# Performance work log

Hardware: AMD Instinct MI355X
Metric: run time of the kernel (lower is better)

The kernel has to match this reference:

```python
import jax, jax.numpy as jnp
import numpy as np

B, T, D = 4096, 200, 128
K_SHORT = 5


def setup_inputs() -> dict:
    key = jax.random.key(0)
    ks = jax.random.split(key, 8)
    hist_items = jax.random.normal(ks[0], (B, T, D), dtype=jnp.float32)
    hist_mask = jax.random.randint(ks[1], (B, T), 0, 2).astype(bool)
    hist_mask = hist_mask.at[:, 0].set(True)  # avoid fully-masked rows
    hist_age_hours = jax.random.uniform(ks[2], (B, T), dtype=jnp.float32) * 168.0
    hist_popularity = jax.random.uniform(ks[3], (B, T), dtype=jnp.float32)
    s = 1.0 / float(np.sqrt(D))
    Wq = jax.random.normal(ks[4], (D, D), dtype=jnp.float32) * s
    Wk = jax.random.normal(ks[5], (D, D), dtype=jnp.float32) * s
    Wv = jax.random.normal(ks[6], (D, D), dtype=jnp.float32) * s
    gate_w = jax.random.normal(ks[7], (1, 2), dtype=jnp.float32) * 0.5
    gate_b = jnp.zeros((1,), dtype=jnp.float32)
    ln_gamma = jnp.ones((D,), dtype=jnp.float32)
    ln_beta = jnp.zeros((D,), dtype=jnp.float32)
    decay_alpha = jnp.asarray(0.05, dtype=jnp.float32)
    return {"hist_items": hist_items, "hist_mask": hist_mask,
            "hist_age_hours": hist_age_hours, "hist_popularity": hist_popularity,
            "Wq": Wq, "Wk": Wk, "Wv": Wv, "gate_w": gate_w, "gate_b": gate_b,
            "ln_gamma": ln_gamma, "ln_beta": ln_beta, "decay_alpha": decay_alpha}


def reference(hist_items, hist_mask, hist_age_hours, hist_popularity,
              Wq, Wk, Wv, gate_w, gate_b, ln_gamma, ln_beta, decay_alpha):
    dt = hist_items.dtype
    maskf = hist_mask.astype(dt)  # (B,T)
    # learnable time-decay bias
    alpha = jax.nn.softplus(decay_alpha) + 1e-6
    decay = jnp.exp(-alpha * hist_age_hours) * maskf  # (B,T)
    # masked mean of history as the single query
    mean_hist = (hist_items * maskf[..., None]).sum(1) / (maskf.sum(1, keepdims=True) + 1e-6)  # (B,D)
    q = mean_hist @ Wq.T                                # (B,D)
    k = jnp.einsum('btd,ed->bte', hist_items, Wk)       # (B,T,D)
    v = jnp.einsum('btd,ed->bte', hist_items, Wv)       # (B,T,D)
    scale = 1.0 / float(np.sqrt(hist_items.shape[-1]))
    scores = jnp.einsum('bd,btd->bt', q, k) * scale + jnp.log(decay + 1e-12)
    scores = jnp.where(hist_mask, scores, -jnp.inf)
    attn = jax.nn.softmax(scores, axis=-1)              # (B,T)
    long_term = jnp.einsum('bt,btd->bd', attn, v)       # (B,D)
    # vectorized last-K window: positions [cnt-K, cnt)
    cnt = jnp.maximum(hist_mask.sum(1), 1)              # (B,) int
    K = min(K_SHORT, hist_items.shape[1])
    ar = jnp.arange(hist_items.shape[1])[None, :]       # (1,T)
    lastk = (ar >= (cnt[:, None] - K)) & (ar < cnt[:, None])  # (B,T) bool
    lk = lastk.astype(dt)
    denom = jnp.maximum(lk.sum(1, keepdims=True), 1.0)  # (B,1)
    short_term = (hist_items * lk[..., None]).sum(1) / denom  # (B,D)
    mean_pop = (hist_popularity * lk).sum(1) / denom[:, 0]
    mean_rec = (hist_age_hours * lk).sum(1) / denom[:, 0]
    ctx = jnp.stack([mean_pop, mean_rec], axis=-1)      # (B,2)
    g = jax.nn.sigmoid(ctx @ gate_w.T + gate_b)         # (B,1)
    user = g * short_term + (1.0 - g) * long_term       # (B,D)
    # LayerNorm (eps=1e-5, biased variance, matching torch)
    mu = user.mean(-1, keepdims=True)
    var = user.var(-1, keepdims=True)
    return (user - mu) / jnp.sqrt(var + 1e-5) * ln_gamma + ln_beta
```

## Files before the change

### kernel.cpp

```cpp
#include <hip/hip_runtime.h>

#define BB 4096
#define TT 200
#define DD 128
#define KSHORT 5

__global__ void detect_mask_kernel(const unsigned* __restrict__ m, int* __restrict__ flag) {
  unsigned bad = 0;
  for (int i = threadIdx.x; i < 1024; i += 64) bad |= (m[i] > 1u) ? 1u : 0u;
  unsigned long long bl = __ballot(bad != 0u);
  if (threadIdx.x == 0) *flag = (bl != 0ULL) ? 1 : 0;
}

__global__ void precompute_A_kernel(const float* __restrict__ Wq,
                                    const float* __restrict__ Wk,
                                    float* __restrict__ A) {
  const int d = blockIdx.x, dp = threadIdx.x;
  float acc = 0.f;
#pragma unroll 8
  for (int e = 0; e < DD; ++e) acc += Wk[e * DD + d] * Wq[e * DD + dp];
  A[d * DD + dp] = acc * 0.08838834764831845f;
}

__global__ __launch_bounds__(256, 4) void k1_stats(
    const float* __restrict__ items, const void* __restrict__ maskp,
    const float* __restrict__ age, const float* __restrict__ pop,
    const float* __restrict__ gate_w, const float* __restrict__ gate_b,
    const float* __restrict__ A, const int* __restrict__ flagp,
    float* __restrict__ qkw, float* __restrict__ shortw, float* __restrict__ gw) {
  __shared__ float s_m[TT];
  __shared__ float s_pm[8 * DD];
  __shared__ float s_ps[8 * DD];
  __shared__ float s_mean[DD];
  __shared__ float s_scal[4];

  const int b = blockIdx.x, tid = threadIdx.x;
  const int lane32 = tid & 31, stream = tid >> 5;
  const int mode = *flagp;

  if (tid < TT) {
    int mk = mode ? (int)((const unsigned char*)maskp)[(size_t)b * TT + tid]
                  : ((const int*)maskp)[(size_t)b * TT + tid];
    s_m[tid] = mk ? 1.f : 0.f;
  }
  __syncthreads();

  if (tid < 64) {
    float c = 0.f;
    for (int t = tid; t < TT; t += 64) c += s_m[t];
#pragma unroll
    for (int o = 32; o > 0; o >>= 1) c += __shfl_xor(c, o);
    if (tid == 0) s_scal[0] = c;
  }
  __syncthreads();

  const float cntf = s_scal[0];
  const int cnt = max((int)(cntf + 0.5f), 1);
  const int lo = max(cnt - KSHORT, 0);
  const float dn = (float)(cnt - lo);

  const float* rowbase = items + (size_t)b * (TT * DD) + lane32 * 4;
  float4 ms = {0.f, 0.f, 0.f, 0.f}, ss = {0.f, 0.f, 0.f, 0.f};
  for (int t = stream; t < TT; t += 8) {
    const float mk = s_m[t];
    const bool inw = (t >= lo) && (t < cnt);
    if (mk > 0.f || inw) {
      float4 v = *(const float4*)(rowbase + t * DD);
      if (mk > 0.f) { ms.x += v.x; ms.y += v.y; ms.z += v.z; ms.w += v.w; }
      if (inw)      { ss.x += v.x; ss.y += v.y; ss.z += v.z; ss.w += v.w; }
    }
  }
  *(float4*)&s_pm[stream * DD + lane32 * 4] = ms;
  *(float4*)&s_ps[stream * DD + lane32 * 4] = ss;
  __syncthreads();

  if (tid < DD) {
    float am = 0.f, as = 0.f;
#pragma unroll
    for (int s = 0; s < 8; ++s) { am += s_pm[s * DD + tid]; as += s_ps[s * DD + tid]; }
    s_mean[tid] = am / (cntf + 1e-6f);
    shortw[(size_t)b * DD + tid] = as / dn;
  } else if (tid == DD) {
    float sp = 0.f, sr = 0.f;
    for (int t = lo; t < cnt; ++t) {
      sp += pop[(size_t)b * TT + t];
      sr += age[(size_t)b * TT + t];
    }
    float z = gate_w[0] * (sp / dn) + gate_w[1] * (sr / dn) + gate_b[0];
    gw[b] = 1.f / (1.f + expf(-z));
  }
  __syncthreads();

  if (tid < DD) {
    const float4* Ar = (const float4*)(A + tid * DD);
    float acc = 0.f;
#pragma unroll
    for (int j = 0; j < DD / 4; ++j) {
      float4 a4 = Ar[j];
      acc += a4.x * s_mean[4 * j] + a4.y * s_mean[4 * j + 1] +
             a4.z * s_mean[4 * j + 2] + a4.w * s_mean[4 * j + 3];
    }
    qkw[(size_t)b * DD + tid] = acc;
  }
}

__global__ __launch_bounds__(256, 4) void k2_attn(
    const float* __restrict__ items, const void* __restrict__ maskp,
    const float* __restrict__ age, const float* __restrict__ Wv,
    const float* __restrict__ gamma, const float* __restrict__ beta,
    const float* __restrict__ alpha_in, const int* __restrict__ flagp,
    const float* __restrict__ qkw, const float* __restrict__ shortw,
    const float* __restrict__ gw, float* __restrict__ out) {
  __shared__ float s_bias[TT];
  __shared__ float s_o[8 * DD];
  __shared__ float s_ml[16];
  __shared__ float s_w[DD];
  __shared__ float s_user[DD];
  __shared__ float s_scal[4];

  const int b = blockIdx.x, tid = threadIdx.x;
  const int lane32 = tid & 31, stream = tid >> 5;
  const int mode = *flagp;

  if (tid < TT) {
    int mk = mode ? (int)((const unsigned char*)maskp)[(size_t)b * TT + tid]
                  : ((const int*)maskp)[(size_t)b * TT + tid];
    const float a = age[(size_t)b * TT + tid];
    const float al = log1pf(expf(alpha_in[0])) + 1e-6f;
    s_bias[tid] = mk ? logf(expf(-al * a) + 1e-12f) : -1e30f;
  }
  __syncthreads();

  const float4 qk = *(const float4*)(qkw + (size_t)b * DD + lane32 * 4);
  const float* rowbase = items + (size_t)b * (TT * DD) + lane32 * 4;

  float m = -1e30f, l = 0.f;
  float4 o = {0.f, 0.f, 0.f, 0.f};
  for (int t = stream; t < TT; t += 8) {
    const float bb = s_bias[t];
    if (bb > -1e29f) {
      float4 v = *(const float4*)(rowbase + t * DD);
      float p = qk.x * v.x + qk.y * v.y + qk.z * v.z + qk.w * v.w;
      p += __shfl_xor(p, 1);
      p += __shfl_xor(p, 2);
      p += __shfl_xor(p, 4);
      p += __shfl_xor(p, 8);
      p += __shfl_xor(p, 16);
      const float s = p + bb;
      const float mn = fmaxf(m, s);
      const float f = __expf(m - mn), e = __expf(s - mn);
      l = l * f + e;
      o.x = o.x * f + e * v.x;
      o.y = o.y * f + e * v.y;
      o.z = o.z * f + e * v.z;
      o.w = o.w * f + e * v.w;
      m = mn;
    }
  }
  *(float4*)&s_o[stream * DD + lane32 * 4] = o;
  if (lane32 == 0) { s_ml[stream * 2] = m; s_ml[stream * 2 + 1] = l; }
  __syncthreads();

  if (tid < DD) {
    float M = s_ml[0];
#pragma unroll
    for (int s = 1; s < 8; ++s) M = fmaxf(M, s_ml[2 * s]);
    float L = 0.f, O = 0.f;
#pragma unroll
    for (int s = 0; s < 8; ++s) {
      const float f = __expf(s_ml[2 * s] - M);
      L += s_ml[2 * s + 1] * f;
      O += s_o[s * DD + tid] * f;
    }
    s_w[tid] = O / L;
  }
  __syncthreads();

  if (tid < DD) {
    const float4* Wr = (const float4*)(Wv + tid * DD);
    float acc = 0.f;
#pragma unroll
    for (int j = 0; j < DD / 4; ++j) {
      float4 a4 = Wr[j];
      acc += a4.x * s_w[4 * j] + a4.y * s_w[4 * j + 1] +
             a4.z * s_w[4 * j + 2] + a4.w * s_w[4 * j + 3];
    }
    const float g = gw[b];
    s_user[tid] = g * shortw[(size_t)b * DD + tid] + (1.f - g) * acc;
  }
  __syncthreads();

  if (tid < 64) {
    const float x0 = s_user[tid], x1 = s_user[64 + tid];
    float su = x0 + x1;
#pragma unroll
    for (int off = 32; off > 0; off >>= 1) su += __shfl_xor(su, off);
    const float mu = su * (1.f / 128.f);
    const float d0 = x0 - mu, d1 = x1 - mu;
    float s2 = d0 * d0 + d1 * d1;
#pragma unroll
    for (int off = 32; off > 0; off >>= 1) s2 += __shfl_xor(s2, off);
    if (tid == 0) {
      s_scal[0] = mu;
      s_scal[1] = 1.f / sqrtf(s2 * (1.f / 128.f) + 1e-5f);
    }
  }
  __syncthreads();

  if (tid < DD) {
    out[(size_t)b * DD + tid] =
        (s_user[tid] - s_scal[0]) * s_scal[1] * gamma[tid] + beta[tid];
  }
}

extern "C" void kernel_launch(void* const* d_in, const int* in_sizes, int n_in,
                              void* d_out, int out_size, void* d_ws, size_t ws_size,
                              hipStream_t stream) {
  const float* items  = (const float*)d_in[0];
  const void*  maskp  = d_in[1];
  const float* age    = (const float*)d_in[2];
  const float* pop    = (const float*)d_in[3];
  const float* Wq     = (const float*)d_in[4];
  const float* Wk     = (const float*)d_in[5];
  const float* Wv     = (const float*)d_in[6];
  const float* gate_w = (const float*)d_in[7];
  const float* gate_b = (const float*)d_in[8];
  const float* gamma  = (const float*)d_in[9];
  const float* beta   = (const float*)d_in[10];
  const float* alpha  = (const float*)d_in[11];

  char* ws = (char*)d_ws;
  int*   flag   = (int*)ws;
  float* A      = (float*)(ws + 256);
  float* qkw    = (float*)(ws + 256 + 65536);
  float* shortw = (float*)(ws + 256 + 65536 + 2097152);
  float* gw     = (float*)(ws + 256 + 65536 + 2 * 2097152);
  float* outp   = (float*)d_out;

  detect_mask_kernel<<<1, 64, 0, stream>>>((const unsigned*)maskp, flag);
  precompute_A_kernel<<<DD, DD, 0, stream>>>(Wq, Wk, A);
  k1_stats<<<BB, 256, 0, stream>>>(items, maskp, age, pop, gate_w, gate_b, A,
                                   flag, qkw, shortw, gw);
  k2_attn<<<BB, 256, 0, stream>>>(items, maskp, age, Wv, gamma, beta, alpha,
                                  flag, qkw, shortw, gw, outp);
}
```

Before: 635.6 us.

## Fuse stats and attention kernels into one per-row kernel with compacted indices

Merges the two per-batch-row kernels into a single kernel, so intermediate q·K weights, short-term vectors and gate values stay in shared memory instead of going through global workspace. Valid time steps are compacted into a shared index list, which removes per-step branch divergence. The softmax drops the running-max rescaling and instead multiplies exp(score) by the precomputed decay factor, replacing log/exp work. The second pass over the row is meant to hit in cache right after the first, but skipping the max subtraction risks overflow if scores get large. The atomic compaction also changes the summation order.

```diff
diff --git a/kernel.cpp b/kernel.cpp
--- a/kernel.cpp
+++ b/kernel.cpp
@@ -22,32 +22,41 @@
   A[d * DD + dp] = acc * 0.08838834764831845f;
 }
 
-__global__ __launch_bounds__(256, 4) void k1_stats(
+__global__ __launch_bounds__(256, 8) void fused_kernel(
     const float* __restrict__ items, const void* __restrict__ maskp,
     const float* __restrict__ age, const float* __restrict__ pop,
-    const float* __restrict__ gate_w, const float* __restrict__ gate_b,
+    const float* __restrict__ Wv, const float* __restrict__ gate_w,
+    const float* __restrict__ gate_b, const float* __restrict__ gamma,
+    const float* __restrict__ beta, const float* __restrict__ alpha_in,
     const float* __restrict__ A, const int* __restrict__ flagp,
-    float* __restrict__ qkw, float* __restrict__ shortw, float* __restrict__ gw) {
-  __shared__ float s_m[TT];
-  __shared__ float s_pm[8 * DD];
-  __shared__ float s_ps[8 * DD];
-  __shared__ float s_mean[DD];
+    float* __restrict__ out) {
+  __shared__ int   s_idx[TT];
+  __shared__ float s_wm[TT], s_ww[TT], s_df[TT];
+  __shared__ float s_pa[8 * DD];
+  __shared__ float s_pb[8 * DD];
+  __shared__ float s_mean[DD], s_qk[DD], s_w[DD], s_user[DD];
+  __shared__ float s_l[8];
   __shared__ float s_scal[4];
+  __shared__ int   s_n;
 
   const int b = blockIdx.x, tid = threadIdx.x;
   const int lane32 = tid & 31, stream = tid >> 5;
   const int mode = *flagp;
 
+  float mymask = 0.f, myage = 0.f;
+  if (tid == 0) s_n = 0;
   if (tid < TT) {
     int mk = mode ? (int)((const unsigned char*)maskp)[(size_t)b * TT + tid]
                   : ((const int*)maskp)[(size_t)b * TT + tid];
-    s_m[tid] = mk ? 1.f : 0.f;
+    mymask = mk ? 1.f : 0.f;
+    myage = age[(size_t)b * TT + tid];
+    s_wm[tid] = mymask;
   }
   __syncthreads();
 
   if (tid < 64) {
     float c = 0.f;
-    for (int t = tid; t < TT; t += 64) c += s_m[t];
+    for (int t = tid; t < TT; t += 64) c += s_wm[t];
 #pragma unroll
     for (int o = 32; o > 0; o >>= 1) c += __shfl_xor(c, o);
     if (tid == 0) s_scal[0] = c;
@@ -59,35 +68,48 @@
   const int lo = max(cnt - KSHORT, 0);
   const float dn = (float)(cnt - lo);
 
+  if (tid < TT) {
+    const bool inw = (tid >= lo) && (tid < cnt);
+    if (mymask > 0.f || inw) {
+      const float al = log1pf(expf(alpha_in[0])) + 1e-6f;
+      const int p = atomicAdd(&s_n, 1);
+      s_idx[p] = tid;
+      s_wm[p] = mymask;
+      s_ww[p] = inw ? 1.f : 0.f;
+      s_df[p] = (mymask > 0.f) ? (__expf(-al * myage) + 1e-12f) : 0.f;
+    }
+  }
+  __syncthreads();
+  const int n = s_n;
+
   const float* rowbase = items + (size_t)b * (TT * DD) + lane32 * 4;
   float4 ms = {0.f, 0.f, 0.f, 0.f}, ss = {0.f, 0.f, 0.f, 0.f};
-  for (int t = stream; t < TT; t += 8) {
-    const float mk = s_m[t];
-    const bool inw = (t >= lo) && (t < cnt);
-    if (mk > 0.f || inw) {
-      float4 v = *(const float4*)(rowbase + t * DD);
-      if (mk > 0.f) { ms.x += v.x; ms.y += v.y; ms.z += v.z; ms.w += v.w; }
-      if (inw)      { ss.x += v.x; ss.y += v.y; ss.z += v.z; ss.w += v.w; }
-    }
-  }
-  *(float4*)&s_pm[stream * DD + lane32 * 4] = ms;
-  *(float4*)&s_ps[stream * DD + lane32 * 4] = ss;
-  __syncthreads();
-
+  for (int i = stream; i < n; i += 8) {
+    const int t = s_idx[i];
+    const float wm = s_wm[i], ww = s_ww[i];
+    const float4 v = *(const float4*)(rowbase + t * DD);
+    ms.x += wm * v.x; ms.y += wm * v.y; ms.z += wm * v.z; ms.w += wm * v.w;
+    ss.x += ww * v.x; ss.y += ww * v.y; ss.z += ww * v.z; ss.w += ww * v.w;
+  }
+  *(float4*)&s_pa[stream * DD + lane32 * 4] = ms;
+  *(float4*)&s_pb[stream * DD + lane32 * 4] = ss;
+  __syncthreads();
+
+  float short_v = 0.f;
   if (tid < DD) {
     float am = 0.f, as = 0.f;
 #pragma unroll
-    for (int s = 0; s < 8; ++s) { am += s_pm[s * DD + tid]; as += s_ps[s * DD + tid]; }
+    for (int s = 0; s < 8; ++s) { am += s_pa[s * DD + tid]; as += s_pb[s * DD + tid]; }
     s_mean[tid] = am / (cntf + 1e-6f);
-    shortw[(size_t)b * DD + tid] = as / dn;
+    short_v = as / dn;
   } else if (tid == DD) {
     float sp = 0.f, sr = 0.f;
     for (int t = lo; t < cnt; ++t) {
       sp += pop[(size_t)b * TT + t];
       sr += age[(size_t)b * TT + t];
     }
-    float z = gate_w[0] * (sp / dn) + gate_w[1] * (sr / dn) + gate_b[0];
-    gw[b] = 1.f / (1.f + expf(-z));
+    const float z = gate_w[0] * (sp / dn) + gate_w[1] * (sr / dn) + gate_b[0];
+    s_scal[1] = 1.f / (1.f + expf(-z));
   }
   __syncthreads();
 
@@ -96,82 +118,42 @@
     float acc = 0.f;
 #pragma unroll
     for (int j = 0; j < DD / 4; ++j) {
-      float4 a4 = Ar[j];
+      const float4 a4 = Ar[j];
       acc += a4.x * s_mean[4 * j] + a4.y * s_mean[4 * j + 1] +
              a4.z * s_mean[4 * j + 2] + a4.w * s_mean[4 * j + 3];
     }
-    qkw[(size_t)b * DD + tid] = acc;
-  }
-}
-
-__global__ __launch_bounds__(256, 4) void k2_attn(
-    const float* __restrict__ items, const void* __restrict__ maskp,
-    const float* __restrict__ age, const float* __restrict__ Wv,
-    const float* __restrict__ gamma, const float* __restrict__ beta,
-    const float* __restrict__ alpha_in, const int* __restrict__ flagp,
-    const float* __restrict__ qkw, const float* __restrict__ shortw,
-    const float* __restrict__ gw, float* __restrict__ out) {
-  __shared__ float s_bias[TT];
-  __shared__ float s_o[8 * DD];
-  __shared__ float s_ml[16];
-  __shared__ float s_w[DD];
-  __shared__ float s_user[DD];
-  __shared__ float s_scal[4];
-
-  const int b = blockIdx.x, tid = threadIdx.x;
-  const int lane32 = tid & 31, stream = tid >> 5;
-  const int mode = *flagp;
-
-  if (tid < TT) {
-    int mk = mode ? (int)((const unsigned char*)maskp)[(size_t)b * TT + tid]
-                  : ((const int*)maskp)[(size_t)b * TT + tid];
-    const float a = age[(size_t)b * TT + tid];
-    const float al = log1pf(expf(alpha_in[0])) + 1e-6f;
-    s_bias[tid] = mk ? logf(expf(-al * a) + 1e-12f) : -1e30f;
-  }
-  __syncthreads();
-
-  const float4 qk = *(const float4*)(qkw + (size_t)b * DD + lane32 * 4);
-  const float* rowbase = items + (size_t)b * (TT * DD) + lane32 * 4;
-
-  float m = -1e30f, l = 0.f;
+    s_qk[tid] = acc;
+  }
+  __syncthreads();
+
+  const float4 qk = *(const float4*)&s_qk[lane32 * 4];
+  float l = 0.f;
   float4 o = {0.f, 0.f, 0.f, 0.f};
-  for (int t = stream; t < TT; t += 8) {
-    const float bb = s_bias[t];
-    if (bb > -1e29f) {
-      float4 v = *(const float4*)(rowbase + t * DD);
-      float p = qk.x * v.x + qk.y * v.y + qk.z * v.z + qk.w * v.w;
-      p += __shfl_xor(p, 1);
-      p += __shfl_xor(p, 2);
-      p += __shfl_xor(p, 4);
-      p += __shfl_xor(p, 8);
-      p += __shfl_xor(p, 16);
-      const float s = p + bb;
-      const float mn = fmaxf(m, s);
-      const float f = __expf(m - mn), e = __expf(s - mn);
-      l = l * f + e;
-      o.x = o.x * f + e * v.x;
-      o.y = o.y * f + e * v.y;
-      o.z = o.z * f + e * v.z;
-      o.w = o.w * f + e * v.w;
-      m = mn;
-    }
-  }
-  *(float4*)&s_o[stream * DD + lane32 * 4] = o;
-  if (lane32 == 0) { s_ml[stream * 2] = m; s_ml[stream * 2 + 1] = l; }
-  __syncthreads();
-
-  if (tid < DD) {
-    float M = s_ml[0];
-#pragma unroll
-    for (int s = 1; s < 8; ++s) M = fmaxf(M, s_ml[2 * s]);
-    float L = 0.f, O = 0.f;
-#pragma unroll
-    for (int s = 0; s < 8; ++s) {
-      const float f = __expf(s_ml[2 * s] - M);
-      L += s_ml[2 * s + 1] * f;
-      O += s_o[s * DD + tid] * f;
-    }
+  for (int i = stream; i < n; i += 8) {
+    const int t = s_idx[i];
+    const float df = s_df[i];
+    const float4 v = *(const float4*)(rowbase + t * DD);
+    float p = qk.x * v.x + qk.y * v.y + qk.z * v.z + qk.w * v.w;
+    p += __shfl_xor(p, 1);
+    p += __shfl_xor(p, 2);
+    p += __shfl_xor(p, 4);
+    p += __shfl_xor(p, 8);
+    p += __shfl_xor(p, 16);
+    const float e = __expf(p) * df;
+    l += e;
+    o.x += e * v.x; o.y += e * v.y; o.z += e * v.z; o.w += e * v.w;
+  }
+  *(float4*)&s_pa[stream * DD + lane32 * 4] = o;
+  if (lane32 == 0) s_l[stream] = l;
+  __syncthreads();
+
+  if (tid < DD) {
+    float O = 0.f;
+#pragma unroll
+    for (int s = 0; s < 8; ++s) O += s_pa[s * DD + tid];
+    float L = 0.f;
+#pragma unroll
+    for (int s = 0; s < 8; ++s) L += s_l[s];
     s_w[tid] = O / L;
   }
   __syncthreads();
@@ -181,12 +163,12 @@
     float acc = 0.f;
 #pragma unroll
     for (int j = 0; j < DD / 4; ++j) {
-      float4 a4 = Wr[j];
+      const float4 a4 = Wr[j];
       acc += a4.x * s_w[4 * j] + a4.y * s_w[4 * j + 1] +
              a4.z * s_w[4 * j + 2] + a4.w * s_w[4 * j + 3];
     }
-    const float g = gw[b];
-    s_user[tid] = g * shortw[(size_t)b * DD + tid] + (1.f - g) * acc;
+    const float g = s_scal[1];
+    s_user[tid] = g * short_v + (1.f - g) * acc;
   }
   __syncthreads();
 
@@ -201,15 +183,15 @@
 #pragma unroll
     for (int off = 32; off > 0; off >>= 1) s2 += __shfl_xor(s2, off);
     if (tid == 0) {
-      s_scal[0] = mu;
-      s_scal[1] = 1.f / sqrtf(s2 * (1.f / 128.f) + 1e-5f);
+      s_scal[2] = mu;
+      s_scal[3] = 1.f / sqrtf(s2 * (1.f / 128.f) + 1e-5f);
     }
   }
   __syncthreads();
 
   if (tid < DD) {
     out[(size_t)b * DD + tid] =
-        (s_user[tid] - s_scal[0]) * s_scal[1] * gamma[tid] + beta[tid];
+        (s_user[tid] - s_scal[2]) * s_scal[3] * gamma[tid] + beta[tid];
   }
 }
 
@@ -230,17 +212,13 @@
   const float* alpha  = (const float*)d_in[11];
 
   char* ws = (char*)d_ws;
-  int*   flag   = (int*)ws;
-  float* A      = (float*)(ws + 256);
-  float* qkw    = (float*)(ws + 256 + 65536);
-  float* shortw = (float*)(ws + 256 + 65536 + 2097152);
-  float* gw     = (float*)(ws + 256 + 65536 + 2 * 2097152);
-  float* outp   = (float*)d_out;
+  int*   flag = (int*)ws;
+  float* A    = (float*)(ws + 256);
+  float* outp = (float*)d_out;
 
   detect_mask_kernel<<<1, 64, 0, stream>>>((const unsigned*)maskp, flag);
   precompute_A_kernel<<<DD, DD, 0, stream>>>(Wq, Wk, A);
-  k1_stats<<<BB, 256, 0, stream>>>(items, maskp, age, pop, gate_w, gate_b, A,
-                                   flag, qkw, shortw, gw);
-  k2_attn<<<BB, 256, 0, stream>>>(items, maskp, age, Wv, gamma, beta, alpha,
-                                  flag, qkw, shortw, gw, outp);
-}
+  fused_kernel<<<BB, 256, 0, stream>>>(items, maskp, age, pop, Wv, gate_w,
+                                       gate_b, gamma, beta, alpha, A, flag,
+                                       outp);
+}
```

Measured after the change: 613.2 us. -3.5%, faster.
